# Kernel optimization log

Measured on AMD Instinct MI355X. Metric: run time of the kernel, lower is better.

Reference implementation:

```python
import jax, jax.numpy as jnp
import numpy as np

B, S, N = 1, 128, 256
D_MSA, D_PAIR, D_HID = 256, 128, 32
EPS = 1e-3
LN_EPS = 1e-5


def _layer_norm(x, w, b):
    mu = jnp.mean(x, axis=-1, keepdims=True)
    var = jnp.mean(jnp.square(x - mu), axis=-1, keepdims=True)
    return (x - mu) * jax.lax.rsqrt(var + LN_EPS) * w + b


def setup_inputs() -> dict:
    key = jax.random.key(0)
    ks = jax.random.split(key, 8)
    sc = lambda fan_in: (1.0 / fan_in) ** 0.5
    return {
        "m": jax.random.normal(ks[0], (B, S, N, D_MSA), dtype=jnp.float32),
        "mask": jnp.ones((B, S, N), dtype=jnp.float32),
        "ln_w": jnp.ones((D_MSA,), dtype=jnp.float32),
        "ln_b": jnp.zeros((D_MSA,), dtype=jnp.float32),
        "w1": jax.random.normal(ks[1], (D_HID, D_MSA), dtype=jnp.float32) * sc(D_MSA),
        "b1": jnp.zeros((D_HID,), dtype=jnp.float32),
        "w2": jax.random.normal(ks[2], (D_HID, D_MSA), dtype=jnp.float32) * sc(D_MSA),
        "b2": jnp.zeros((D_HID,), dtype=jnp.float32),
        "w_out": jax.random.normal(ks[3], (D_PAIR, D_HID * D_HID), dtype=jnp.float32) * sc(D_HID * D_HID),
        "b_out": jnp.zeros((D_PAIR,), dtype=jnp.float32),
        "ln_out_w": jnp.ones((D_PAIR,), dtype=jnp.float32),
        "ln_out_b": jnp.zeros((D_PAIR,), dtype=jnp.float32),
        "wz": jax.random.normal(ks[4], (D_PAIR, D_PAIR), dtype=jnp.float32) * sc(D_PAIR),
        "bz": jnp.zeros((D_PAIR,), dtype=jnp.float32),
    }


def reference(m, mask, ln_w, ln_b, w1, b1, w2, b2, w_out, b_out, ln_out_w, ln_out_b, wz, bz):
    # m: [B, S, N, d_msa], mask: [B, S, N]
    x = _layer_norm(m, ln_w, ln_b)
    n_res = mask.shape[-1]
    mk = mask[..., None] * (n_res ** -0.5)          # [B, S, N, 1] (layer_norm_out branch)
    a = (jnp.einsum('bsnd,hd->bsnh', x, w1) + b1) * mk
    b_ = (jnp.einsum('bsnd,hd->bsnh', x, w2) + b2) * mk
    a = jnp.swapaxes(a, -2, -3)                      # [B, N, S, h]
    b_ = jnp.swapaxes(b_, -2, -3)                    # [B, N, S, h]
    outer = jnp.einsum('bisc,bjse->bijce', a, b_)    # [B, N, N, h, h]
    outer = outer.reshape(outer.shape[:-2] + (-1,))  # [B, N, N, h*h]
    z = jnp.einsum('bijk,pk->bijp', outer, w_out) + b_out  # [B, N, N, d_pair]
    norm = jnp.einsum('bsi,bsj->bij', mk[..., 0], mk[..., 0])[..., None]
    z = z / (EPS + norm)
    z = jax.nn.gelu(z, approximate=False)
    z = _layer_norm(z, ln_out_w, ln_out_b)
    z = jnp.einsum('bijp,qp->bijq', z, wz) + bz
    return z
```

## Files before the change

kernel.cpp:

```cpp
#include <hip/hip_runtime.h>
#include <hip/hip_bf16.h>
#include <math.h>

#define EPSC 1e-3f

typedef __attribute__((ext_vector_type(8)))  short  short8;
typedef __attribute__((ext_vector_type(4)))  float  float4v;
typedef __attribute__((ext_vector_type(16))) float  float16v;

static __device__ __forceinline__ unsigned short f2bf(float f) {
    union { float f; unsigned u; } x; x.f = f;
    unsigned r = x.u + 0x7FFFu + ((x.u >> 16) & 1u);
    return (unsigned short)(r >> 16);
}
static __device__ __forceinline__ unsigned pk_bf16(float lo, float hi) {
    union { __hip_bfloat162 h; unsigned u; } cv;
    cv.h = __float22bfloat162_rn(make_float2(lo, hi));
    return cv.u;
}
static __device__ __forceinline__ float4v mfma16(short8 a, short8 b, float4v c) {
    return __builtin_amdgcn_mfma_f32_16x16x32_bf16(a, b, c, 0, 0, 0);
}
static __device__ __forceinline__ float16v mfma32(short8 a, short8 b, float16v c) {
    return __builtin_amdgcn_mfma_f32_32x32x16_bf16(a, b, c, 0, 0, 0);
}

#define OFF_NORM 0ull
#define OFF_AT   262144ull
#define OFF_BT   2359296ull
#define OFF_WOF  4456448ull
#define OFF_WZF  4718592ull
#define OFF_W12  4751360ull

__global__ __launch_bounds__(256) void k_pre(
    const float* __restrict__ m, const float* __restrict__ mask,
    const float* __restrict__ ln_w, const float* __restrict__ ln_b,
    const float* __restrict__ w1, const float* __restrict__ b1,
    const float* __restrict__ w2, const float* __restrict__ b2,
    const float* __restrict__ w_out, const float* __restrict__ wz,
    unsigned short* __restrict__ aT, unsigned short* __restrict__ bT,
    unsigned short* __restrict__ wobF, unsigned short* __restrict__ wzF,
    const unsigned short* __restrict__ w12F_in,
    unsigned short* __restrict__ w12F,
    float* __restrict__ normw)
{
    __shared__ unsigned short xs[64 * 266];
    __shared__ unsigned short tr[64 * 76];
    __shared__ float mkl[64];
    __shared__ float b12[64];
    int t = threadIdx.x;
    int b = blockIdx.x;

    if (b >= 1152) {
        int i = b - 1152, j = t;
        float acc = 0.f;
#pragma unroll 8
        for (int s = 0; s < 128; ++s)
            acc += mask[s * 256 + i] * mask[s * 256 + j];
        normw[i * 256 + j] = acc * (1.0f / 256.0f);
        return;
    }
    if (b >= 512) {
        int idx = (b - 512) * 256 + t;
        if (idx < 131072) {
            int j = idx & 7, lane = (idx >> 3) & 63, k16 = (idx >> 9) & 31;
            int kh = (idx >> 14) & 1, pw = (idx >> 15) & 3;
            int p = pw * 32 + (lane & 31);
            int k = kh * 512 + k16 * 16 + (lane >> 5) * 8 + j;
            wobF[idx] = f2bf(w_out[p * 1024 + k]);
        } else if (idx < 147456) {
            int q = idx - 131072;
            int j = q & 7, lane = (q >> 3) & 63, kk = (q >> 9) & 3, w = q >> 11;
            int p = w * 16 + (lane & 15);
            int k = kk * 32 + (lane >> 4) * 8 + j;
            wzF[q] = f2bf(wz[p * 128 + k]);
        } else if (idx < 163840) {
            int q = idx - 147456;
            int j = q & 7, lane = (q >> 3) & 63, ht = (q >> 9) & 3, kk = q >> 11;
            int h = ht * 16 + (lane & 15);
            int d = kk * 32 + (lane >> 4) * 8 + j;
            w12F[q] = f2bf(h < 32 ? w1[h * 256 + d] : w2[(h - 32) * 256 + d]);
        }
        return;
    }

    int w = t >> 6, lane = t & 63;
    int g = lane >> 4, l15 = lane & 15;
    int rr = lane >> 4, l16 = lane & 15;
    int n0 = (b & 31) * 8, s0 = (b >> 5) * 8;

    if (t < 64) {
        b12[t] = (t < 32) ? b1[t] : b2[t - 32];
        mkl[t] = mask[(s0 + (t >> 3)) * 256 + n0 + (t & 7)] * 0.0625f;
    }

    float4 lw4[4], lb4[4];
#pragma unroll
    for (int q = 0; q < 4; ++q) {
        lw4[q] = *(const float4*)(ln_w + q * 64 + l16 * 4);
        lb4[q] = *(const float4*)(ln_b + q * 64 + l16 * 4);
    }

#pragma unroll
    for (int pass = 0; pass < 4; ++pass) {
        int r = w * 16 + pass * 4 + rr;
        const float* src = m + ((size_t)(s0 + (r >> 3)) * 256 + n0 + (r & 7)) * 256;
        float4 v[4];
#pragma unroll
        for (int q = 0; q < 4; ++q)
            v[q] = *(const float4*)(src + q * 64 + l16 * 4);
        float sum = 0.f, sq = 0.f;
#pragma unroll
        for (int q = 0; q < 4; ++q) {
            sum += v[q].x + v[q].y + v[q].z + v[q].w;
            sq  += v[q].x * v[q].x + v[q].y * v[q].y + v[q].z * v[q].z + v[q].w * v[q].w;
        }
#pragma unroll
        for (int mm = 1; mm <= 8; mm <<= 1) {
            sum += __shfl_xor(sum, mm);
            sq  += __shfl_xor(sq, mm);
        }
        float mu = sum * (1.f / 256.f);
        float rstd = rsqrtf(sq * (1.f / 256.f) - mu * mu + 1e-5f);
#pragma unroll
        for (int q = 0; q < 4; ++q) {
            uint2 u;
            u.x = pk_bf16((v[q].x - mu) * rstd * lw4[q].x + lb4[q].x,
                          (v[q].y - mu) * rstd * lw4[q].y + lb4[q].y);
            u.y = pk_bf16((v[q].z - mu) * rstd * lw4[q].z + lb4[q].z,
                          (v[q].w - mu) * rstd * lw4[q].w + lb4[q].w);
            *(uint2*)(xs + r * 266 + q * 64 + l16 * 4) = u;
        }
    }
    __syncthreads();

    float4v zf4 = {0.f, 0.f, 0.f, 0.f};
    float4v acc[4]; acc[0] = zf4; acc[1] = zf4; acc[2] = zf4; acc[3] = zf4;
#pragma unroll
    for (int kk = 0; kk < 8; ++kk) {
        short8 af = *(const short8*)(xs + (w * 16 + l15) * 266 + kk * 32 + g * 8);
#pragma unroll
        for (int ht = 0; ht < 4; ++ht) {
            short8 bfr = *(const short8*)(w12F_in + ((size_t)(kk * 4 + ht) * 64 + lane) * 8);
            acc[ht] = mfma16(af, bfr, acc[ht]);
        }
    }
#pragma unroll
    for (int ht = 0; ht < 4; ++ht) {
        int h = ht * 16 + l15;
        float bias = b12[h];
        int rbase = w * 16 + g * 4;
        uint2 u;
        u.x = pk_bf16((acc[ht][0] + bias) * mkl[rbase + 0], (acc[ht][1] + bias) * mkl[rbase + 1]);
        u.y = pk_bf16((acc[ht][2] + bias) * mkl[rbase + 2], (acc[ht][3] + bias) * mkl[rbase + 3]);
        *(uint2*)(tr + h * 76 + rbase) = u;
    }
    __syncthreads();

#pragma unroll
    for (int it = 0; it < 2; ++it) {
        int q = t + it * 256;
        int h = q >> 3, n_l = q & 7;
        unsigned short vv[8];
#pragma unroll
        for (int s_l = 0; s_l < 8; ++s_l)
            vv[s_l] = tr[h * 76 + s_l * 8 + n_l];
        uint4 u;
        u.x = (unsigned)vv[0] | ((unsigned)vv[1] << 16);
        u.y = (unsigned)vv[2] | ((unsigned)vv[3] << 16);
        u.z = (unsigned)vv[4] | ((unsigned)vv[5] << 16);
        u.w = (unsigned)vv[6] | ((unsigned)vv[7] << 16);
        int row = n_l * 32 + (h & 31);
        int dwcol = (s0 >> 1) ^ ((row & 7) << 2);
        unsigned short* dst = ((h < 32) ? aT : bT)
            + (size_t)(n0 >> 3) * 32768 + row * 128 + dwcol * 2;
        *(uint4*)dst = u;
    }
}

__global__ __launch_bounds__(512, 2) void k2_fused(
    const unsigned short* __restrict__ aT, const unsigned short* __restrict__ bT,
    const unsigned short* __restrict__ wobF, const unsigned short* __restrict__ wzF,
    const float* __restrict__ b_out, const float* __restrict__ normw,
    const float* __restrict__ ln_ow, const float* __restrict__ ln_ob,
    const float* __restrict__ bz, float* __restrict__ out)
{
    __shared__ char smem[131072];
    unsigned* s32 = (unsigned*)smem;
    unsigned* oL = (unsigned*)smem;
    float* zA = (float*)smem;
    float* zB = (float*)(smem + 33792);
    unsigned short* lnL = (unsigned short*)(smem + 67584);

    int t = threadIdx.x;
    int w = t >> 6, lane = t & 63;
    int g = lane >> 4, l15 = lane & 15;
    int bj = blockIdx.x, bi = blockIdx.y;
    int wn = w & 1, wm = w >> 1;

    {
        const uint4* Agv = (const uint4*)(aT + (size_t)bi * 32768);
        const uint4* Bgv = (const uint4*)(bT + (size_t)bj * 32768);
#pragma unroll
        for (int it = 0; it < 8; ++it) {
            int q = t + it * 512;
            *(uint4*)(s32 + q * 4) = Agv[q];
            *(uint4*)(s32 + 16384 + q * 4) = Bgv[q];
        }
    }
    __syncthreads();

    float4v zf4 = {0.f, 0.f, 0.f, 0.f};
    float4v acc[4][8];
#pragma unroll
    for (int fm = 0; fm < 4; ++fm)
#pragma unroll
        for (int fn = 0; fn < 8; ++fn) acc[fm][fn] = zf4;

    {
        int sw = (l15 & 7) << 2;
#pragma unroll
        for (int kk = 0; kk < 4; ++kk) {
            int col = (kk * 16 + g * 4) ^ sw;
            short8 af[4], bf[8];
#pragma unroll
            for (int fm = 0; fm < 4; ++fm) {
                int row = wm * 64 + fm * 16 + l15;
                af[fm] = *(const short8*)((const char*)(s32 + row * 64 + col));
            }
#pragma unroll
            for (int fn = 0; fn < 8; ++fn) {
                int row = wn * 128 + fn * 16 + l15;
                bf[fn] = *(const short8*)((const char*)(s32 + 16384 + row * 64 + col));
            }
#pragma unroll
            for (int fm = 0; fm < 4; ++fm)
#pragma unroll
                for (int fn = 0; fn < 8; ++fn)
                    acc[fm][fn] = mfma16(bf[fn], af[fm], acc[fm][fn]);
        }
    }
    __syncthreads();

#pragma unroll
    for (int fm = 0; fm < 4; ++fm) {
#pragma unroll
        for (int fn = 0; fn < 8; ++fn) {
            int pair = (wm * 2 + (fm >> 1)) * 8 + wn * 4 + (fn >> 1);
            int c = (fm & 1) * 16 + l15;
            int o = (fn & 1) * 8 + 2 * g;
            int off = c * 16 + o;
            int dw = pair * 512 + (off ^ ((((pair & 7) ^ (off >> 6)) & 7) << 2));
            float4v a4 = acc[fm][fn];
            uint2 u;
            u.x = pk_bf16(a4[0], a4[1]);
            u.y = pk_bf16(a4[2], a4[3]);
            *(uint2*)(oL + dw) = u;
        }
    }
    __syncthreads();

    {
        int pw = w >> 1, kh = w & 1;
        int l31 = lane & 31, h2 = lane >> 5;
        float16v accA = {0.f};
        float16v accB = {0.f};
        const unsigned short* wbase = wobF + (size_t)w * 16384;
#pragma unroll 8
        for (int k16 = 0; k16 < 32; ++k16) {
            int kg = kh * 32 + k16;
            int off = kg * 8 + h2 * 4;
            int dws = off ^ ((((l31 & 7) ^ (off >> 6)) & 7) << 2);
            short8 b2 = *(const short8*)(wbase + (size_t)(k16 * 64 + lane) * 8);
            short8 aA = *(const short8*)(oL + l31 * 512 + dws);
            short8 aB = *(const short8*)(oL + (32 + l31) * 512 + dws);
            accA = mfma32(aA, b2, accA);
            accB = mfma32(aB, b2, accB);
        }
        __syncthreads();
        float* zdst = kh ? zB : zA;
#pragma unroll
        for (int reg = 0; reg < 16; ++reg) {
            int pr = (reg & 3) + 8 * (reg >> 2) + 4 * h2;
            zdst[pr * 132 + pw * 32 + l31] = accA[reg];
            zdst[(32 + pr) * 132 + pw * 32 + l31] = accB[reg];
        }
    }
    __syncthreads();

    {
        const float4 loA = *(const float4*)(ln_ow + l15 * 8);
        const float4 loB = *(const float4*)(ln_ow + l15 * 8 + 4);
        const float4 lbA = *(const float4*)(ln_ob + l15 * 8);
        const float4 lbB = *(const float4*)(ln_ob + l15 * 8 + 4);
        const float4 boA = *(const float4*)(b_out + l15 * 8);
        const float4 boB = *(const float4*)(b_out + l15 * 8 + 4);
        float lw8[8] = {loA.x, loA.y, loA.z, loA.w, loB.x, loB.y, loB.z, loB.w};
        float lb8[8] = {lbA.x, lbA.y, lbA.z, lbA.w, lbB.x, lbB.y, lbB.z, lbB.w};
        float bo8[8] = {boA.x, boA.y, boA.z, boA.w, boB.x, boB.y, boB.z, boB.w};
#pragma unroll
        for (int it = 0; it < 2; ++it) {
            int pair = w * 8 + it * 4 + g;
            int iG = bi * 8 + (pair >> 3), jG = bj * 8 + (pair & 7);
            float inv = 1.0f / (EPSC + normw[iG * 256 + jG]);
            float4v zA0 = *(const float4v*)(zA + pair * 132 + l15 * 8);
            float4v zA1 = *(const float4v*)(zA + pair * 132 + l15 * 8 + 4);
            float4v zB0 = *(const float4v*)(zB + pair * 132 + l15 * 8);
            float4v zB1 = *(const float4v*)(zB + pair * 132 + l15 * 8 + 4);
            float vals[8];
            float sum = 0.f, sq = 0.f;
#pragma unroll
            for (int e2 = 0; e2 < 8; ++e2) {
                float v = ((e2 < 4) ? (zA0[e2] + zB0[e2]) : (zA1[e2 - 4] + zB1[e2 - 4])) + bo8[e2];
                v *= inv;
                v = 0.5f * v * (1.0f + erff(v * 0.70710678118654752f));
                vals[e2] = v; sum += v; sq += v * v;
            }
#pragma unroll
            for (int mm = 1; mm <= 8; mm <<= 1) {
                sum += __shfl_xor(sum, mm);
                sq  += __shfl_xor(sq, mm);
            }
            float mu = sum * (1.0f / 128.0f);
            float rstd = rsqrtf(sq * (1.0f / 128.0f) - mu * mu + 1e-5f);
            uint4 upk;
            upk.x = pk_bf16((vals[0] - mu) * rstd * lw8[0] + lb8[0],
                            (vals[1] - mu) * rstd * lw8[1] + lb8[1]);
            upk.y = pk_bf16((vals[2] - mu) * rstd * lw8[2] + lb8[2],
                            (vals[3] - mu) * rstd * lw8[3] + lb8[3]);
            upk.z = pk_bf16((vals[4] - mu) * rstd * lw8[4] + lb8[4],
                            (vals[5] - mu) * rstd * lw8[5] + lb8[5]);
            upk.w = pk_bf16((vals[6] - mu) * rstd * lw8[6] + lb8[6],
                            (vals[7] - mu) * rstd * lw8[7] + lb8[7]);
            *(uint4*)(lnL + pair * 136 + l15 * 8) = upk;
        }
    }
    __syncthreads();

    {
        float4v acc3[4]; acc3[0] = zf4; acc3[1] = zf4; acc3[2] = zf4; acc3[3] = zf4;
#pragma unroll
        for (int kk = 0; kk < 4; ++kk) {
            short8 bfw = *(const short8*)(wzF + ((size_t)(w * 4 + kk) * 64 + lane) * 8);
#pragma unroll
            for (int fr = 0; fr < 4; ++fr) {
                short8 af3 = *(const short8*)(lnL + (fr * 16 + l15) * 136 + kk * 32 + g * 8);
                acc3[fr] = mfma16(af3, bfw, acc3[fr]);
            }
        }
        float bzq = bz[w * 16 + l15];
#pragma unroll
        for (int fr = 0; fr < 4; ++fr) {
#pragma unroll
            for (int r = 0; r < 4; ++r) {
                int pair = fr * 16 + g * 4 + r;
                int row = (bi * 8 + (pair >> 3)) * 256 + bj * 8 + (pair & 7);
                out[(size_t)row * 128 + w * 16 + l15] = acc3[fr][r] + bzq;
            }
        }
    }
}

extern "C" void kernel_launch(void* const* d_in, const int* in_sizes, int n_in,
                              void* d_out, int out_size, void* d_ws, size_t ws_size,
                              hipStream_t stream) {
    const float* m      = (const float*)d_in[0];
    const float* mask   = (const float*)d_in[1];
    const float* ln_w   = (const float*)d_in[2];
    const float* ln_b   = (const float*)d_in[3];
    const float* w1     = (const float*)d_in[4];
    const float* b1     = (const float*)d_in[5];
    const float* w2     = (const float*)d_in[6];
    const float* b2     = (const float*)d_in[7];
    const float* w_out  = (const float*)d_in[8];
    const float* b_out  = (const float*)d_in[9];
    const float* ln_ow  = (const float*)d_in[10];
    const float* ln_ob  = (const float*)d_in[11];
    const float* wz     = (const float*)d_in[12];
    const float* bz     = (const float*)d_in[13];
    float* out = (float*)d_out;
    char*  ws  = (char*)d_ws;

    float* normw          = (float*)(ws + OFF_NORM);
    unsigned short* aTb   = (unsigned short*)(ws + OFF_AT);
    unsigned short* bTb   = (unsigned short*)(ws + OFF_BT);
    unsigned short* wobF  = (unsigned short*)(ws + OFF_WOF);
    unsigned short* wzF   = (unsigned short*)(ws + OFF_WZF);
    unsigned short* w12F  = (unsigned short*)(ws + OFF_W12);

    {
        struct L {
            static __global__ void __launch_bounds__(256) cvt12(
                const float* __restrict__ w1, const float* __restrict__ w2,
                unsigned short* __restrict__ w12F) {
                int q = blockIdx.x * 256 + threadIdx.x;
                int j = q & 7, lane = (q >> 3) & 63, ht = (q >> 9) & 3, kk = q >> 11;
                int h = ht * 16 + (lane & 15);
                int d = kk * 32 + (lane >> 4) * 8 + j;
                w12F[q] = f2bf(h < 32 ? w1[h * 256 + d] : w2[(h - 32) * 256 + d]);
            }
        };
        L::cvt12<<<dim3(64), dim3(256), 0, stream>>>(w1, w2, w12F);
    }
    k_pre<<<dim3(1408), dim3(256), 0, stream>>>(m, mask, ln_w, ln_b, w1, b1, w2, b2,
                                                w_out, wz, aTb, bTb, wobF, wzF,
                                                w12F, w12F, normw);
    k2_fused<<<dim3(32, 32), dim3(512), 0, stream>>>(aTb, bTb, wobF, wzF, b_out, normw,
                                                     ln_ow, ln_ob, bz, out);
}
```

Measured before the change: 166.2 us.

## Halve k2 shared memory via K-split staging and two-pass epilogue; drop w12 pre-kernel

The fused outer-product kernel now stages the A/B tiles in two K halves and processes the w_out projection, GELU/LayerNorm and wz projection in two passes of 32 pairs each, cutting LDS from 128KB to 64KB so more blocks can be resident per CU. The separate w1/w2 bf16 conversion kernel is removed, and k_pre instead reads fp32 w1/w2 directly and converts them in registers. This saves one launch and raises occupancy, at the cost of extra barriers, redundant weight loads and conversions per block, and repeated wz loads across passes.

```diff
diff --git a/kernel.cpp b/kernel.cpp
--- a/kernel.cpp
+++ b/kernel.cpp
@@ -30,7 +30,6 @@
 #define OFF_BT   2359296ull
 #define OFF_WOF  4456448ull
 #define OFF_WZF  4718592ull
-#define OFF_W12  4751360ull
 
 __global__ __launch_bounds__(256) void k_pre(
     const float* __restrict__ m, const float* __restrict__ mask,
@@ -40,8 +39,6 @@
     const float* __restrict__ w_out, const float* __restrict__ wz,
     unsigned short* __restrict__ aT, unsigned short* __restrict__ bT,
     unsigned short* __restrict__ wobF, unsigned short* __restrict__ wzF,
-    const unsigned short* __restrict__ w12F_in,
-    unsigned short* __restrict__ w12F,
     float* __restrict__ normw)
 {
     __shared__ unsigned short xs[64 * 266];
@@ -51,8 +48,8 @@
     int t = threadIdx.x;
     int b = blockIdx.x;
 
-    if (b >= 1152) {
-        int i = b - 1152, j = t;
+    if (b >= 1088) {
+        int i = b - 1088, j = t;
         float acc = 0.f;
 #pragma unroll 8
         for (int s = 0; s < 128; ++s)
@@ -68,18 +65,12 @@
             int p = pw * 32 + (lane & 31);
             int k = kh * 512 + k16 * 16 + (lane >> 5) * 8 + j;
             wobF[idx] = f2bf(w_out[p * 1024 + k]);
-        } else if (idx < 147456) {
+        } else {
             int q = idx - 131072;
             int j = q & 7, lane = (q >> 3) & 63, kk = (q >> 9) & 3, w = q >> 11;
             int p = w * 16 + (lane & 15);
             int k = kk * 32 + (lane >> 4) * 8 + j;
             wzF[q] = f2bf(wz[p * 128 + k]);
-        } else if (idx < 163840) {
-            int q = idx - 147456;
-            int j = q & 7, lane = (q >> 3) & 63, ht = (q >> 9) & 3, kk = q >> 11;
-            int h = ht * 16 + (lane & 15);
-            int d = kk * 32 + (lane >> 4) * 8 + j;
-            w12F[q] = f2bf(h < 32 ? w1[h * 256 + d] : w2[(h - 32) * 256 + d]);
         }
         return;
     }
@@ -141,8 +132,16 @@
         short8 af = *(const short8*)(xs + (w * 16 + l15) * 266 + kk * 32 + g * 8);
 #pragma unroll
         for (int ht = 0; ht < 4; ++ht) {
-            short8 bfr = *(const short8*)(w12F_in + ((size_t)(kk * 4 + ht) * 64 + lane) * 8);
-            acc[ht] = mfma16(af, bfr, acc[ht]);
+            int h = ht * 16 + l15;
+            const float* wr = (h < 32) ? (w1 + h * 256) : (w2 + (h - 32) * 256);
+            float4 wa = *(const float4*)(wr + kk * 32 + g * 8);
+            float4 wb = *(const float4*)(wr + kk * 32 + g * 8 + 4);
+            union { short8 s; unsigned u[4]; } bfr;
+            bfr.u[0] = pk_bf16(wa.x, wa.y);
+            bfr.u[1] = pk_bf16(wa.z, wa.w);
+            bfr.u[2] = pk_bf16(wb.x, wb.y);
+            bfr.u[3] = pk_bf16(wb.z, wb.w);
+            acc[ht] = mfma16(af, bfr.s, acc[ht]);
         }
     }
 #pragma unroll
@@ -185,12 +184,12 @@
     const float* __restrict__ ln_ow, const float* __restrict__ ln_ob,
     const float* __restrict__ bz, float* __restrict__ out)
 {
-    __shared__ char smem[131072];
+    __shared__ char smem[65536];
     unsigned* s32 = (unsigned*)smem;
     unsigned* oL = (unsigned*)smem;
     float* zA = (float*)smem;
-    float* zB = (float*)(smem + 33792);
-    unsigned short* lnL = (unsigned short*)(smem + 67584);
+    float* zB = (float*)(smem + 16896);
+    unsigned short* lnL = (unsigned short*)(smem + 33792);
 
     int t = threadIdx.x;
     int w = t >> 6, lane = t & 63;
@@ -198,17 +197,8 @@
     int bj = blockIdx.x, bi = blockIdx.y;
     int wn = w & 1, wm = w >> 1;
 
-    {
-        const uint4* Agv = (const uint4*)(aT + (size_t)bi * 32768);
-        const uint4* Bgv = (const uint4*)(bT + (size_t)bj * 32768);
-#pragma unroll
-        for (int it = 0; it < 8; ++it) {
-            int q = t + it * 512;
-            *(uint4*)(s32 + q * 4) = Agv[q];
-            *(uint4*)(s32 + 16384 + q * 4) = Bgv[q];
-        }
-    }
-    __syncthreads();
+    const unsigned* Ag = (const unsigned*)(aT + (size_t)bi * 32768);
+    const unsigned* Bg = (const unsigned*)(bT + (size_t)bj * 32768);
 
     float4v zf4 = {0.f, 0.f, 0.f, 0.f};
     float4v acc[4][8];
@@ -217,22 +207,28 @@
 #pragma unroll
         for (int fn = 0; fn < 8; ++fn) acc[fm][fn] = zf4;
 
-    {
+    for (int kh = 0; kh < 2; ++kh) {
+        if (kh) __syncthreads();
+#pragma unroll
+        for (int it = 0; it < 4; ++it) {
+            int idx = t + it * 512;
+            int row = idx >> 3, c4 = idx & 7;
+            int off = (c4 * 4) ^ ((row & 7) << 2);
+            *(uint4*)(s32 + row * 32 + off) = *(const uint4*)(Ag + row * 64 + kh * 32 + off);
+            *(uint4*)(s32 + 8192 + row * 32 + off) = *(const uint4*)(Bg + row * 64 + kh * 32 + off);
+        }
+        __syncthreads();
         int sw = (l15 & 7) << 2;
 #pragma unroll
-        for (int kk = 0; kk < 4; ++kk) {
-            int col = (kk * 16 + g * 4) ^ sw;
+        for (int kk2 = 0; kk2 < 2; ++kk2) {
+            int col = (kk2 * 16 + g * 4) ^ sw;
             short8 af[4], bf[8];
 #pragma unroll
-            for (int fm = 0; fm < 4; ++fm) {
-                int row = wm * 64 + fm * 16 + l15;
-                af[fm] = *(const short8*)((const char*)(s32 + row * 64 + col));
-            }
-#pragma unroll
-            for (int fn = 0; fn < 8; ++fn) {
-                int row = wn * 128 + fn * 16 + l15;
-                bf[fn] = *(const short8*)((const char*)(s32 + 16384 + row * 64 + col));
-            }
+            for (int fm = 0; fm < 4; ++fm)
+                af[fm] = *(const short8*)((const char*)(s32 + (wm * 64 + fm * 16 + l15) * 32 + col));
+#pragma unroll
+            for (int fn = 0; fn < 8; ++fn)
+                bf[fn] = *(const short8*)((const char*)(s32 + 8192 + (wn * 128 + fn * 16 + l15) * 32 + col));
 #pragma unroll
             for (int fm = 0; fm < 4; ++fm)
 #pragma unroll
@@ -240,73 +236,72 @@
                     acc[fm][fn] = mfma16(bf[fn], af[fm], acc[fm][fn]);
         }
     }
-    __syncthreads();
-
-#pragma unroll
-    for (int fm = 0; fm < 4; ++fm) {
-#pragma unroll
-        for (int fn = 0; fn < 8; ++fn) {
-            int pair = (wm * 2 + (fm >> 1)) * 8 + wn * 4 + (fn >> 1);
-            int c = (fm & 1) * 16 + l15;
-            int o = (fn & 1) * 8 + 2 * g;
-            int off = c * 16 + o;
-            int dw = pair * 512 + (off ^ ((((pair & 7) ^ (off >> 6)) & 7) << 2));
-            float4v a4 = acc[fm][fn];
-            uint2 u;
-            u.x = pk_bf16(a4[0], a4[1]);
-            u.y = pk_bf16(a4[2], a4[3]);
-            *(uint2*)(oL + dw) = u;
-        }
-    }
-    __syncthreads();
-
-    {
-        int pw = w >> 1, kh = w & 1;
-        int l31 = lane & 31, h2 = lane >> 5;
-        float16v accA = {0.f};
-        float16v accB = {0.f};
-        const unsigned short* wbase = wobF + (size_t)w * 16384;
+
+    const float4 loA = *(const float4*)(ln_ow + l15 * 8);
+    const float4 loB = *(const float4*)(ln_ow + l15 * 8 + 4);
+    const float4 lbA = *(const float4*)(ln_ob + l15 * 8);
+    const float4 lbB = *(const float4*)(ln_ob + l15 * 8 + 4);
+    const float4 boA = *(const float4*)(b_out + l15 * 8);
+    const float4 boB = *(const float4*)(b_out + l15 * 8 + 4);
+    float lw8[8] = {loA.x, loA.y, loA.z, loA.w, loB.x, loB.y, loB.z, loB.w};
+    float lb8[8] = {lbA.x, lbA.y, lbA.z, lbA.w, lbB.x, lbB.y, lbB.z, lbB.w};
+    float bo8[8] = {boA.x, boA.y, boA.z, boA.w, boB.x, boB.y, boB.z, boB.w};
+    float bzq = bz[w * 16 + l15];
+
+    for (int p = 0; p < 2; ++p) {
+        __syncthreads();
+        if ((wm >> 1) == p) {
+#pragma unroll
+            for (int fm = 0; fm < 4; ++fm) {
+#pragma unroll
+                for (int fn = 0; fn < 8; ++fn) {
+                    int pl = ((wm & 1) * 2 + (fm >> 1)) * 8 + wn * 4 + (fn >> 1);
+                    int c = (fm & 1) * 16 + l15;
+                    int o = (fn & 1) * 8 + 2 * g;
+                    int off = c * 16 + o;
+                    int dw = pl * 512 + (off ^ ((((pl & 7) ^ (off >> 6)) & 7) << 2));
+                    float4v a4 = acc[fm][fn];
+                    uint2 u;
+                    u.x = pk_bf16(a4[0], a4[1]);
+                    u.y = pk_bf16(a4[2], a4[3]);
+                    *(uint2*)(oL + dw) = u;
+                }
+            }
+        }
+        __syncthreads();
+
+        {
+            int kh = w & 1, pw = w >> 1;
+            int l31 = lane & 31, h2 = lane >> 5;
+            float16v a32 = {0.f};
+            const unsigned short* wbase = wobF + (size_t)w * 16384;
 #pragma unroll 8
-        for (int k16 = 0; k16 < 32; ++k16) {
-            int kg = kh * 32 + k16;
-            int off = kg * 8 + h2 * 4;
-            int dws = off ^ ((((l31 & 7) ^ (off >> 6)) & 7) << 2);
-            short8 b2 = *(const short8*)(wbase + (size_t)(k16 * 64 + lane) * 8);
-            short8 aA = *(const short8*)(oL + l31 * 512 + dws);
-            short8 aB = *(const short8*)(oL + (32 + l31) * 512 + dws);
-            accA = mfma32(aA, b2, accA);
-            accB = mfma32(aB, b2, accB);
-        }
-        __syncthreads();
-        float* zdst = kh ? zB : zA;
-#pragma unroll
-        for (int reg = 0; reg < 16; ++reg) {
-            int pr = (reg & 3) + 8 * (reg >> 2) + 4 * h2;
-            zdst[pr * 132 + pw * 32 + l31] = accA[reg];
-            zdst[(32 + pr) * 132 + pw * 32 + l31] = accB[reg];
-        }
-    }
-    __syncthreads();
-
-    {
-        const float4 loA = *(const float4*)(ln_ow + l15 * 8);
-        const float4 loB = *(const float4*)(ln_ow + l15 * 8 + 4);
-        const float4 lbA = *(const float4*)(ln_ob + l15 * 8);
-        const float4 lbB = *(const float4*)(ln_ob + l15 * 8 + 4);
-        const float4 boA = *(const float4*)(b_out + l15 * 8);
-        const float4 boB = *(const float4*)(b_out + l15 * 8 + 4);
-        float lw8[8] = {loA.x, loA.y, loA.z, loA.w, loB.x, loB.y, loB.z, loB.w};
-        float lb8[8] = {lbA.x, lbA.y, lbA.z, lbA.w, lbB.x, lbB.y, lbB.z, lbB.w};
-        float bo8[8] = {boA.x, boA.y, boA.z, boA.w, boB.x, boB.y, boB.z, boB.w};
-#pragma unroll
-        for (int it = 0; it < 2; ++it) {
-            int pair = w * 8 + it * 4 + g;
-            int iG = bi * 8 + (pair >> 3), jG = bj * 8 + (pair & 7);
+            for (int k16 = 0; k16 < 32; ++k16) {
+                int kg = kh * 32 + k16;
+                int off = kg * 8 + h2 * 4;
+                int dws = off ^ ((((l31 & 7) ^ (off >> 6)) & 7) << 2);
+                short8 b2 = *(const short8*)(wbase + (size_t)(k16 * 64 + lane) * 8);
+                short8 aA = *(const short8*)(oL + l31 * 512 + dws);
+                a32 = mfma32(aA, b2, a32);
+            }
+            __syncthreads();
+            float* zdst = kh ? zB : zA;
+#pragma unroll
+            for (int reg = 0; reg < 16; ++reg) {
+                int pr = (reg & 3) + 8 * (reg >> 2) + 4 * h2;
+                zdst[pr * 132 + pw * 32 + l31] = a32[reg];
+            }
+        }
+        __syncthreads();
+
+        {
+            int pl = w * 4 + g;
+            int iG = bi * 8 + p * 4 + (pl >> 3), jG = bj * 8 + (pl & 7);
             float inv = 1.0f / (EPSC + normw[iG * 256 + jG]);
-            float4v zA0 = *(const float4v*)(zA + pair * 132 + l15 * 8);
-            float4v zA1 = *(const float4v*)(zA + pair * 132 + l15 * 8 + 4);
-            float4v zB0 = *(const float4v*)(zB + pair * 132 + l15 * 8);
-            float4v zB1 = *(const float4v*)(zB + pair * 132 + l15 * 8 + 4);
+            float4v zA0 = *(const float4v*)(zA + pl * 132 + l15 * 8);
+            float4v zA1 = *(const float4v*)(zA + pl * 132 + l15 * 8 + 4);
+            float4v zB0 = *(const float4v*)(zB + pl * 132 + l15 * 8);
+            float4v zB1 = *(const float4v*)(zB + pl * 132 + l15 * 8 + 4);
             float vals[8];
             float sum = 0.f, sq = 0.f;
 #pragma unroll
@@ -332,30 +327,29 @@
                             (vals[5] - mu) * rstd * lw8[5] + lb8[5]);
             upk.w = pk_bf16((vals[6] - mu) * rstd * lw8[6] + lb8[6],
                             (vals[7] - mu) * rstd * lw8[7] + lb8[7]);
-            *(uint4*)(lnL + pair * 136 + l15 * 8) = upk;
-        }
-    }
-    __syncthreads();
-
-    {
-        float4v acc3[4]; acc3[0] = zf4; acc3[1] = zf4; acc3[2] = zf4; acc3[3] = zf4;
-#pragma unroll
-        for (int kk = 0; kk < 4; ++kk) {
-            short8 bfw = *(const short8*)(wzF + ((size_t)(w * 4 + kk) * 64 + lane) * 8);
-#pragma unroll
-            for (int fr = 0; fr < 4; ++fr) {
-                short8 af3 = *(const short8*)(lnL + (fr * 16 + l15) * 136 + kk * 32 + g * 8);
-                acc3[fr] = mfma16(af3, bfw, acc3[fr]);
-            }
-        }
-        float bzq = bz[w * 16 + l15];
-#pragma unroll
-        for (int fr = 0; fr < 4; ++fr) {
-#pragma unroll
-            for (int r = 0; r < 4; ++r) {
-                int pair = fr * 16 + g * 4 + r;
-                int row = (bi * 8 + (pair >> 3)) * 256 + bj * 8 + (pair & 7);
-                out[(size_t)row * 128 + w * 16 + l15] = acc3[fr][r] + bzq;
+            *(uint4*)(lnL + pl * 136 + l15 * 8) = upk;
+        }
+        __syncthreads();
+
+        {
+            float4v acc3[2]; acc3[0] = zf4; acc3[1] = zf4;
+#pragma unroll
+            for (int kk = 0; kk < 4; ++kk) {
+                short8 bfw = *(const short8*)(wzF + ((size_t)(w * 4 + kk) * 64 + lane) * 8);
+#pragma unroll
+                for (int fr = 0; fr < 2; ++fr) {
+                    short8 af3 = *(const short8*)(lnL + (fr * 16 + l15) * 136 + kk * 32 + g * 8);
+                    acc3[fr] = mfma16(af3, bfw, acc3[fr]);
+                }
+            }
+#pragma unroll
+            for (int fr = 0; fr < 2; ++fr) {
+#pragma unroll
+                for (int r = 0; r < 4; ++r) {
+                    int pl = fr * 16 + g * 4 + r;
+                    int row = (bi * 8 + p * 4 + (pl >> 3)) * 256 + bj * 8 + (pl & 7);
+                    out[(size_t)row * 128 + w * 16 + l15] = acc3[fr][r] + bzq;
+                }
             }
         }
     }
@@ -386,25 +380,9 @@
     unsigned short* bTb   = (unsigned short*)(ws + OFF_BT);
     unsigned short* wobF  = (unsigned short*)(ws + OFF_WOF);
     unsigned short* wzF   = (unsigned short*)(ws + OFF_WZF);
-    unsigned short* w12F  = (unsigned short*)(ws + OFF_W12);
-
-    {
-        struct L {
-            static __global__ void __launch_bounds__(256) cvt12(
-                const float* __restrict__ w1, const float* __restrict__ w2,
-                unsigned short* __restrict__ w12F) {
-                int q = blockIdx.x * 256 + threadIdx.x;
-                int j = q & 7, lane = (q >> 3) & 63, ht = (q >> 9) & 3, kk = q >> 11;
-                int h = ht * 16 + (lane & 15);
-                int d = kk * 32 + (lane >> 4) * 8 + j;
-                w12F[q] = f2bf(h < 32 ? w1[h * 256 + d] : w2[(h - 32) * 256 + d]);
-            }
-        };
-        L::cvt12<<<dim3(64), dim3(256), 0, stream>>>(w1, w2, w12F);
-    }
-    k_pre<<<dim3(1408), dim3(256), 0, stream>>>(m, mask, ln_w, ln_b, w1, b1, w2, b2,
-                                                w_out, wz, aTb, bTb, wobF, wzF,
-                                                w12F, w12F, normw);
+
+    k_pre<<<dim3(1344), dim3(256), 0, stream>>>(m, mask, ln_w, ln_b, w1, b1, w2, b2,
+                                                w_out, wz, aTb, bTb, wobF, wzF, normw);
     k2_fused<<<dim3(32, 32), dim3(512), 0, stream>>>(aTb, bTb, wobF, wzF, b_out, normw,
                                                      ln_ow, ln_ob, bz, out);
 }
```

Result: slower. 188.3 us (+13.3%).
